# Kernel optimization log

Hardware: AMD Instinct MI355X
Metric: run time of the kernel (lower is better)

## Reference

```python
import jax, jax.numpy as jnp
import numpy as np

B, T, N, D, H, MH = 4, 16, 128, 16, 64, 128  # batch, timesteps, nodes, n_in_node, n_hid, msg_hid


def setup_inputs() -> dict:
    key = jax.random.key(0)
    ks = jax.random.split(key, 24)
    s = 0.1
    inp = {
        'A': jax.random.uniform(ks[0], (B, N, N), dtype=jnp.float32),
        'X': jax.random.normal(ks[1], (B, T, N, D), dtype=jnp.float32),
        'W_msg1': s * jax.random.normal(ks[2], (2 * H, MH), dtype=jnp.float32),
        'b_msg1': s * jax.random.normal(ks[3], (MH,), dtype=jnp.float32),
        'W_msg2': s * jax.random.normal(ks[4], (MH, H), dtype=jnp.float32),
        'b_msg2': s * jax.random.normal(ks[5], (H,), dtype=jnp.float32),
        'W_ir': s * jax.random.normal(ks[6], (D, H), dtype=jnp.float32),
        'b_ir': s * jax.random.normal(ks[7], (H,), dtype=jnp.float32),
        'W_ii': s * jax.random.normal(ks[8], (D, H), dtype=jnp.float32),
        'b_ii': s * jax.random.normal(ks[9], (H,), dtype=jnp.float32),
        'W_in': s * jax.random.normal(ks[10], (D, H), dtype=jnp.float32),
        'b_in': s * jax.random.normal(ks[11], (H,), dtype=jnp.float32),
        'W_hr': s * jax.random.normal(ks[12], (H, H), dtype=jnp.float32),
        'W_hi': s * jax.random.normal(ks[13], (H, H), dtype=jnp.float32),
        'W_hh': s * jax.random.normal(ks[14], (H, H), dtype=jnp.float32),
        'W_o1': s * jax.random.normal(ks[15], (H, H), dtype=jnp.float32),
        'b_o1': s * jax.random.normal(ks[16], (H,), dtype=jnp.float32),
        'W_o2': s * jax.random.normal(ks[17], (H, H), dtype=jnp.float32),
        'b_o2': s * jax.random.normal(ks[18], (H,), dtype=jnp.float32),
        'W_o3': s * jax.random.normal(ks[19], (H, D), dtype=jnp.float32),
        'b_o3': s * jax.random.normal(ks[20], (D,), dtype=jnp.float32),
        'log_sigma': jnp.log(jnp.float32(0.1)),
    }
    return inp


def reference(A, X, W_msg1, b_msg1, W_msg2, b_msg2, W_ir, b_ir, W_ii, b_ii,
              W_in, b_in, W_hr, W_hi, W_hh, W_o1, b_o1, W_o2, b_o2, W_o3,
              b_o3, log_sigma):
    Bv, Tv, Nv, Dv = X.shape
    Hv = W_hr.shape[0]
    # project_adjacency: symmetrize, zero diag, clamp to [0,1]
    A = (A + jnp.swapaxes(A, -1, -2)) * 0.5
    A = A * (1.0 - jnp.eye(Nv, dtype=A.dtype))
    A = jnp.clip(A, 0.0, 1.0)
    # split msg_fc1 into sender / receiver halves (cat([senders, receivers]) @ W)
    W1s, W1r = W_msg1[:Hv], W_msg1[Hv:]

    def step(carry, xs):
        hidden, total = carry
        x_t, x_next = xs  # [B,N,D]
        # message passing on hidden state: msg1[b,i,j] = tanh(h_i@W1s + h_j@W1r + b)
        hs = hidden @ W1s                      # [B,N,MH] sender part
        hr = hidden @ W1r + b_msg1             # [B,N,MH] receiver part
        m1 = jnp.tanh(hs[:, :, None, :] + hr[:, None, :, :])  # [B,N,N,MH]
        msg = jnp.tanh(m1 @ W_msg2 + b_msg2)   # [B,N,N,H]
        # weight by soft adjacency, sum over senders i -> agg at receiver j
        agg = jnp.einsum('bij,bijh->bjh', A, msg)  # [B,N,H]
        # GRU-style gating
        r = jax.nn.sigmoid(x_t @ W_ir + b_ir + agg @ W_hr)
        i = jax.nn.sigmoid(x_t @ W_ii + b_ii + agg @ W_hi)
        n = jnp.tanh(x_t @ W_in + b_in + r * (agg @ W_hh))
        hidden_new = (1.0 - i) * n + i * hidden
        # output MLP with residual
        p1 = jax.nn.relu(hidden_new @ W_o1 + b_o1)
        p2 = jax.nn.relu(p1 @ W_o2 + b_o2)
        pred = x_t + (p2 @ W_o3 + b_o3)
        # gaussian log-likelihood
        sigma = jnp.exp(log_sigma)
        mse = jnp.sum((x_next - pred) ** 2)
        const = Nv * Dv * Bv * jnp.log(sigma * jnp.sqrt(2.0 * jnp.pi))
        total = total - (mse / (2.0 * sigma ** 2) + const)
        return (hidden_new, total), pred

    hidden0 = jnp.zeros((Bv, Nv, Hv), dtype=X.dtype)
    xs = (jnp.swapaxes(X[:, :-1], 0, 1), jnp.swapaxes(X[:, 1:], 0, 1))  # time-major
    (_, loglik), preds = jax.lax.scan(step, (hidden0, jnp.float32(0.0)), xs)
    X_pred = jnp.swapaxes(preds, 0, 1)  # [B, T-1, N, D]
    return X_pred, loglik
```

## Files before the change

### kernel.cpp

```cpp
#include <hip/hip_runtime.h>

#define NBLK 512
#define CSCALE 2.8853900817779268f

#define OFF_HS   0
#define OFF_PART 65536
#define OFF_SYNC 66048
#define OFF_BF   66560

#define BW2F  0
#define BWIR  8192
#define BWII  9216
#define BWIN  10240
#define BWHR  11264
#define BWHI  15360
#define BWHH  19456
#define BWO1  23552
#define BWO2  27648
#define BWO3  31744
#define BW1S  32768
#define BW1RT 49152

#define INIT_TOTAL (32768 + 512 + 49152 + 8192)

typedef __attribute__((ext_vector_type(8))) __bf16 bf16x8;
typedef __attribute__((ext_vector_type(4))) float f32x4;
union frag_u { bf16x8 v; unsigned short s[8]; int4 q; };
union ldu { int4 q; unsigned short s[8]; unsigned u[4]; };

__device__ __forceinline__ unsigned short f2b(float x) {
  unsigned int u = __float_as_uint(x);
  u += 0x7fffu + ((u >> 16) & 1u);
  return (unsigned short)(u >> 16);
}
__device__ __forceinline__ float b2f(unsigned short u) {
  return __uint_as_float(((unsigned int)u) << 16);
}
__device__ __forceinline__ float fast_tanh(float x) {
  float e = __builtin_amdgcn_exp2f(x * CSCALE);
  return 1.0f - 2.0f * __builtin_amdgcn_rcpf(e + 1.0f);
}
__device__ __forceinline__ float tanh_pre(float x) {
  float e = __builtin_amdgcn_exp2f(x);
  return 1.0f - 2.0f * __builtin_amdgcn_rcpf(e + 1.0f);
}
__device__ __forceinline__ float fast_sigmoid(float x) {
  float e = __builtin_amdgcn_exp2f(x * -1.4426950408889634f);
  return __builtin_amdgcn_rcpf(1.0f + e);
}
__device__ __forceinline__ unsigned pack_bf2(float lo, float hi) {
  unsigned a = __float_as_uint(lo) + 0x8000u;
  unsigned b = __float_as_uint(hi) + 0x8000u;
  return __builtin_amdgcn_perm(b, a, 0x07060302u);
}
__device__ __forceinline__ void st_coh_u32(unsigned* p, unsigned v) {
  __hip_atomic_store(p, v, __ATOMIC_RELAXED, __HIP_MEMORY_SCOPE_AGENT);
}
__device__ __forceinline__ void st_coh_i32(int* p, int v) {
  __hip_atomic_store(p, v, __ATOMIC_RELAXED, __HIP_MEMORY_SCOPE_AGENT);
}

__global__ void init_kernel(const float* __restrict__ W_msg2,
                            const float* __restrict__ W_ir, const float* __restrict__ W_ii,
                            const float* __restrict__ W_in,
                            const float* __restrict__ W_hr, const float* __restrict__ W_hi,
                            const float* __restrict__ W_hh,
                            const float* __restrict__ W_o1, const float* __restrict__ W_o2,
                            const float* __restrict__ W_o3,
                            const float* __restrict__ W_msg1, float* __restrict__ ws) {
  int idx = blockIdx.x * 256 + threadIdx.x;
  unsigned short* bw = (unsigned short*)(ws + OFF_BF);
  if (idx < 32768) { ws[OFF_HS + idx] = 0.0f; return; }
  idx -= 32768;
  if (idx < 512) { ((int*)(ws + OFF_SYNC))[idx] = 0; return; }
  idx -= 512;
  if (idx < 8192) {
    int f = idx >> 9, l = (idx >> 3) & 63, jj = idx & 7;
    int kc = f >> 2, nt = f & 3;
    int k = kc * 32 + ((l >> 4) << 3) + jj;
    int n = (nt << 4) + (l & 15);
    bw[BW2F + idx] = f2b(W_msg2[k * 64 + n] * CSCALE);
    return;
  }
  idx -= 8192;
  if (idx < 1024) { bw[BWIR + idx] = f2b(W_ir[idx]); return; }
  idx -= 1024;
  if (idx < 1024) { bw[BWII + idx] = f2b(W_ii[idx]); return; }
  idx -= 1024;
  if (idx < 1024) { bw[BWIN + idx] = f2b(W_in[idx]); return; }
  idx -= 1024;
  if (idx < 4096) { bw[BWHR + idx] = f2b(W_hr[idx]); return; }
  idx -= 4096;
  if (idx < 4096) { bw[BWHI + idx] = f2b(W_hi[idx]); return; }
  idx -= 4096;
  if (idx < 4096) { bw[BWHH + idx] = f2b(W_hh[idx]); return; }
  idx -= 4096;
  if (idx < 4096) { bw[BWO1 + idx] = f2b(W_o1[idx]); return; }
  idx -= 4096;
  if (idx < 4096) { bw[BWO2 + idx] = f2b(W_o2[idx]); return; }
  idx -= 4096;
  if (idx < 1024) { bw[BWO3 + idx] = f2b(W_o3[idx]); return; }
  idx -= 1024;
  if (idx < 16384) { bw[BW1S + idx] = f2b(W_msg1[idx]); return; }
  idx -= 16384;
  if (idx < 8192) {
    int m = idx >> 6, h = idx & 63;
    bw[BW1RT + idx] = f2b(W_msg1[(64 + h) * 128 + m]);
    return;
  }
}

__launch_bounds__(256, 2)
__global__ void step_all_kernel(const float* __restrict__ A, const float* __restrict__ X,
                                const float* __restrict__ b_msg1, const float* __restrict__ b_msg2,
                                const float* __restrict__ b_ir, const float* __restrict__ b_ii,
                                const float* __restrict__ b_in,
                                const float* __restrict__ b_o1, const float* __restrict__ b_o2,
                                const float* __restrict__ b_o3,
                                float* __restrict__ ws, float* __restrict__ out) {
  const int tid = threadIdx.x;
  const int bj = blockIdx.x;
  const int b = bj >> 7, j = bj & 127;
  const int wave = tid >> 6, lane = tid & 63;
  const unsigned short* bw = (const unsigned short*)(ws + OFF_BF);
  unsigned short* hs16 = (unsigned short*)(ws + OFF_HS);
  int* flags = (int*)(ws + OFF_SYNC);

  __shared__ __align__(16) unsigned short lds_gate_t[12288];
  __shared__ __align__(16) unsigned short lds_w1t[8192];
  __shared__ __align__(16) unsigned short lds_outt[9216];
  __shared__ __align__(16) float sh_hr[128];
  __shared__ __align__(16) float sh_Ar[128];
  __shared__ __align__(16) float sh_aggw[4][64];
  __shared__ __align__(16) float sh_agg[64];
  __shared__ __align__(16) float sh_xall[256];
  __shared__ __align__(16) float sh_hid[64];
  __shared__ __align__(16) float sh_hist[960];
  __shared__ __align__(16) float sh_pre[4][64];
  __shared__ int sh_w01;

  for (int i = tid; i < 12288; i += 256) {
    int g = i >> 12, r = i & 4095, c = r >> 8, rem = r & 255, h = rem >> 2, s = rem & 3;
    lds_gate_t[i] = bw[BWHR + (g << 12) + (((c << 2) + s) << 6) + h];
  }
  for (int i = tid; i < 8192; i += 256) {
    int c = i >> 9, rem = i & 511, m = rem >> 2, s = rem & 3;
    lds_w1t[i] = bw[BW1S + (((c << 2) + s) << 7) + m];
  }
  for (int i = tid; i < 8192; i += 256) {
    int o = i >> 12, r = i & 4095, c = r >> 8, rem = r & 255, h = rem >> 2, s = rem & 3;
    lds_outt[i] = bw[BWO1 + (o << 12) + (((c << 2) + s) << 6) + h];
  }
  for (int i = tid; i < 1024; i += 256) {
    int c = i >> 6, rem = i & 63, d = rem >> 2, s = rem & 3;
    lds_outt[8192 + i] = bw[BWO3 + (((c << 2) + s) << 4) + d];
  }
  {
    int t0 = tid >> 4, d = tid & 15;
    sh_xall[tid] = X[(((b << 4) + t0) << 11) + (j << 4) + d];
  }
  if (tid < 128) {
    float a1 = A[(b << 14) + (j << 7) + tid];
    float a2 = A[(b << 14) + (tid << 7) + j];
    float v = 0.5f * (a1 + a2);
    v = (tid == j) ? 0.0f : v;
    sh_Ar[tid] = fminf(fmaxf(v, 0.0f), 1.0f);
    sh_hr[tid] = b_msg1[tid] * CSCALE;
  } else if (tid < 192) {
    sh_hid[tid - 128] = 0.0f;
  }
  if (tid == 0) sh_w01 = 0;

  frag_u Bf[16];
  const int4* bw2 = (const int4*)bw;
#pragma unroll
  for (int f = 0; f < 16; ++f) Bf[f].q = bw2[f * 64 + lane];
  float b2v[4];
#pragma unroll
  for (int nt = 0; nt < 4; ++nt) b2v[nt] = b_msg2[nt * 16 + (lane & 15)] * CSCALE;
  float my_bias = 0.0f;
  float wx[16];
  if (wave != 2) {
    my_bias = (wave == 0) ? b_ir[lane] : (wave == 1) ? b_ii[lane] : b_in[lane];
    const int xo = (wave == 0) ? BWIR : (wave == 1) ? BWII : BWIN;
#pragma unroll
    for (int d = 0; d < 16; ++d) wx[d] = b2f(bw[xo + d * 64 + lane]);
  }
  const float bm1a = b_msg1[lane], bm1b = b_msg1[lane + 64];
  const float bo1 = b_o1[lane], bo2 = b_o2[lane];
  const float bo3 = (lane < 16) ? b_o3[lane] : 0.0f;
  float macc = 0.0f;

  const int lane15 = lane & 15;
  const int k0 = (lane >> 4) << 3;
  __syncthreads();

  for (int t = 0; t < 15; ++t) {
    const int par = t & 1;
    const unsigned short* hs_cur = hs16 + par * 65536;
    unsigned short* hs_nxt = hs16 + (par ^ 1) * 65536;

    ldu va[8];
    {
      const unsigned short* p0 = hs_cur + (((b << 7) + (wave << 5) + lane15) << 7) + k0;
      const unsigned short* p1 = p0 + 2048;
      asm volatile(
          "global_load_dwordx4 %0, %8, off sc0 sc1\n\t"
          "global_load_dwordx4 %1, %8, off offset:64 sc0 sc1\n\t"
          "global_load_dwordx4 %2, %8, off offset:128 sc0 sc1\n\t"
          "global_load_dwordx4 %3, %8, off offset:192 sc0 sc1\n\t"
          "global_load_dwordx4 %4, %9, off sc0 sc1\n\t"
          "global_load_dwordx4 %5, %9, off offset:64 sc0 sc1\n\t"
          "global_load_dwordx4 %6, %9, off offset:128 sc0 sc1\n\t"
          "global_load_dwordx4 %7, %9, off offset:192 sc0 sc1\n\t"
          "s_waitcnt vmcnt(0)"
          : "=&v"(va[0].q), "=&v"(va[1].q), "=&v"(va[2].q), "=&v"(va[3].q),
            "=&v"(va[4].q), "=&v"(va[5].q), "=&v"(va[6].q), "=&v"(va[7].q)
          : "v"(p0), "v"(p1)
          : "memory");
    }

    float part[4] = {0.f, 0.f, 0.f, 0.f};
#pragma unroll
    for (int c = 0; c < 2; ++c) {
      f32x4 acc[4];
#pragma unroll
      for (int nt = 0; nt < 4; ++nt) acc[nt] = (f32x4){0.f, 0.f, 0.f, 0.f};
#pragma unroll
      for (int kc = 0; kc < 4; ++kc) {
        const ldu& u = va[c * 4 + kc];
        const float* hp = sh_hr + kc * 32 + k0;
        frag_u Af;
        int* ap = (int*)&Af.q;
#pragma unroll
        for (int p = 0; p < 4; ++p) {
          unsigned w = u.u[p];
          float x0 = __uint_as_float(w << 16) + hp[2 * p];
          float x1 = __uint_as_float(w & 0xffff0000u) + hp[2 * p + 1];
          ap[p] = (int)pack_bf2(tanh_pre(x0), tanh_pre(x1));
        }
#pragma unroll
        for (int nt = 0; nt < 4; ++nt)
          acc[nt] = __builtin_amdgcn_mfma_f32_16x16x32_bf16(Af.v, Bf[kc * 4 + nt].v, acc[nt], 0, 0, 0);
      }
      const int ibase = ((wave << 1) + c) << 4;
      float4 aw = *(const float4*)(sh_Ar + ibase + ((lane >> 4) << 2));
#pragma unroll
      for (int r = 0; r < 4; ++r) {
        float wv = (r == 0) ? aw.x : (r == 1) ? aw.y : (r == 2) ? aw.z : aw.w;
#pragma unroll
        for (int nt = 0; nt < 4; ++nt)
          part[nt] += wv * tanh_pre(acc[nt][r] + b2v[nt]);
      }
    }
#pragma unroll
    for (int nt = 0; nt < 4; ++nt) {
      part[nt] += __shfl_xor(part[nt], 16);
      part[nt] += __shfl_xor(part[nt], 32);
    }
    if (lane < 16) {
#pragma unroll
      for (int nt = 0; nt < 4; ++nt) sh_aggw[wave][nt * 16 + lane] = part[nt];
    }
    __syncthreads();
    if (tid < 64)
      sh_agg[tid] = sh_aggw[0][tid] + sh_aggw[1][tid] + sh_aggw[2][tid] + sh_aggw[3][tid];
    __syncthreads();

    {
      float s = 0.0f;
      if (wave != 2) {
        s = my_bias;
        const float4* xr = (const float4*)(sh_xall + (t << 4));
#pragma unroll
        for (int c = 0; c < 4; ++c) {
          float4 xv = xr[c];
          s += xv.x * wx[4 * c] + xv.y * wx[4 * c + 1] + xv.z * wx[4 * c + 2] + xv.w * wx[4 * c + 3];
        }
      }
      if (wave != 3) {
        const ushort4* gp = ((const ushort4*)lds_gate_t) + (wave << 10) + lane;
        const float4* ag = (const float4*)sh_agg;
        float a0 = s, a1 = 0.f, a2 = 0.f, a3 = 0.f;
#pragma unroll
        for (int c = 0; c < 16; ++c) {
          ushort4 wv = gp[c << 6];
          float4 av = ag[c];
          a0 += av.x * b2f(wv.x); a1 += av.y * b2f(wv.y);
          a2 += av.z * b2f(wv.z); a3 += av.w * b2f(wv.w);
        }
        s = (a0 + a1) + (a2 + a3);
      }
      sh_pre[wave][lane] = s;
    }
    __syncthreads();
    if (tid < 64) {
      float r  = fast_sigmoid(sh_pre[0][tid]);
      float ig = fast_sigmoid(sh_pre[1][tid]);
      float n  = fast_tanh(sh_pre[3][tid] + r * sh_pre[2][tid]);
      float hnew = (1.0f - ig) * n + ig * sh_hid[tid];
      sh_hid[tid] = hnew;
      sh_hist[t * 64 + tid] = hnew;
    }
    __syncthreads();

    if (t < 14) {
      if (wave <= 1) {
        const int m = tid;
        const ushort4* wp = ((const ushort4*)lds_w1t) + m;
        const float4* h4 = (const float4*)sh_hid;
        float a0 = 0.f, a1 = 0.f, a2 = 0.f, a3 = 0.f;
#pragma unroll
        for (int c = 0; c < 16; ++c) {
          ushort4 wv = wp[c << 7];
          float4 hv = h4[c];
          a0 += hv.x * b2f(wv.x); a1 += hv.y * b2f(wv.y);
          a2 += hv.z * b2f(wv.z); a3 += hv.w * b2f(wv.w);
        }
        float s = ((a0 + a1) + (a2 + a3)) * CSCALE;
        float hi = __shfl_down(s, 1);
        if (!(lane & 1))
          st_coh_u32((unsigned*)hs_nxt + (bj << 6) + (m >> 1), pack_bf2(s, hi));
        asm volatile("s_waitcnt vmcnt(0)" ::: "memory");
        if (lane == 0) atomicAdd(&sh_w01, 1);
        if (wave == 0) {
          const int tgt = t + 1;
          if (lane == 0) {
            while (__hip_atomic_load(&sh_w01, __ATOMIC_RELAXED, __HIP_MEMORY_SCOPE_WORKGROUP) < 2 * tgt) {}
            st_coh_i32(flags + (b << 7) + j, tgt);
          }
          const int* fp = flags + (b << 7) + (lane << 1);
          int2 fv;
          for (;;) {
            asm volatile("global_load_dwordx2 %0, %1, off sc0 sc1\n\ts_waitcnt vmcnt(0)"
                         : "=v"(fv) : "v"(fp) : "memory");
            if (!__any(fv.x < tgt || fv.y < tgt)) break;
            __builtin_amdgcn_s_sleep(1);
          }
        }
      } else if (wave == 2) {
        const int4* wp1 = (const int4*)(bw + BW1RT + (lane << 6));
        const int4* wp2 = (const int4*)(bw + BW1RT + ((lane + 64) << 6));
        const float4* h4 = (const float4*)sh_hid;
        float s1a = bm1a, s1b = 0.f, s2a = bm1b, s2b = 0.f;
#pragma unroll
        for (int c = 0; c < 8; ++c) {
          ldu u1, u2; u1.q = wp1[c]; u2.q = wp2[c];
          float4 h0 = h4[2 * c], h1 = h4[2 * c + 1];
          s1a += h0.x * b2f(u1.s[0]); s1b += h0.y * b2f(u1.s[1]);
          s1a += h0.z * b2f(u1.s[2]); s1b += h0.w * b2f(u1.s[3]);
          s1a += h1.x * b2f(u1.s[4]); s1b += h1.y * b2f(u1.s[5]);
          s1a += h1.z * b2f(u1.s[6]); s1b += h1.w * b2f(u1.s[7]);
          s2a += h0.x * b2f(u2.s[0]); s2b += h0.y * b2f(u2.s[1]);
          s2a += h0.z * b2f(u2.s[2]); s2b += h0.w * b2f(u2.s[3]);
          s2a += h1.x * b2f(u2.s[4]); s2b += h1.y * b2f(u2.s[5]);
          s2a += h1.z * b2f(u2.s[6]); s2b += h1.w * b2f(u2.s[7]);
        }
        sh_hr[lane] = (s1a + s1b) * CSCALE;
        sh_hr[lane + 64] = (s2a + s2b) * CSCALE;
      }
    }
    __syncthreads();
  }

#pragma unroll
  for (int it = 0; it < 4; ++it) {
    const int tt = wave + it * 4;
    if (tt >= 15) continue;
    const float4* h4 = (const float4*)(sh_hist + tt * 64);
    {
      const ushort4* r1 = ((const ushort4*)lds_outt) + lane;
      float a0 = bo1, a1 = 0.f, a2 = 0.f, a3 = 0.f;
#pragma unroll
      for (int c = 0; c < 16; ++c) {
        ushort4 wv = r1[c << 6]; float4 hv = h4[c];
        a0 += hv.x * b2f(wv.x); a1 += hv.y * b2f(wv.y);
        a2 += hv.z * b2f(wv.z); a3 += hv.w * b2f(wv.w);
      }
      sh_pre[wave][lane] = fmaxf((a0 + a1) + (a2 + a3), 0.0f);
    }
    {
      const ushort4* r2 = ((const ushort4*)lds_outt) + 1024 + lane;
      const float4* p4 = (const float4*)sh_pre[wave];
      float a0 = bo2, a1 = 0.f, a2 = 0.f, a3 = 0.f;
#pragma unroll
      for (int c = 0; c < 16; ++c) {
        ushort4 wv = r2[c << 6]; float4 pv = p4[c];
        a0 += pv.x * b2f(wv.x); a1 += pv.y * b2f(wv.y);
        a2 += pv.z * b2f(wv.z); a3 += pv.w * b2f(wv.w);
      }
      sh_aggw[wave][lane] = fmaxf((a0 + a1) + (a2 + a3), 0.0f);
    }
    if (lane < 16) {
      const ushort4* r3 = ((const ushort4*)lds_outt) + 2048 + lane;
      const float4* q4 = (const float4*)sh_aggw[wave];
      float a0 = bo3, a1 = 0.f, a2 = 0.f, a3 = 0.f;
#pragma unroll
      for (int c = 0; c < 16; ++c) {
        ushort4 wv = r3[c << 4]; float4 qv = q4[c];
        a0 += qv.x * b2f(wv.x); a1 += qv.y * b2f(wv.y);
        a2 += qv.z * b2f(wv.z); a3 += qv.w * b2f(wv.w);
      }
      float pred = sh_xall[(tt << 4) + lane] + (a0 + a1) + (a2 + a3);
      out[((b * 15 + tt) * 128 + j) * 16 + lane] = pred;
      float d = sh_xall[((tt + 1) << 4) + lane] - pred;
      macc += d * d;
    }
  }
  macc += __shfl_xor(macc, 1);
  macc += __shfl_xor(macc, 2);
  macc += __shfl_xor(macc, 4);
  macc += __shfl_xor(macc, 8);
  __syncthreads();
  if (lane == 0) sh_agg[wave] = macc;
  __syncthreads();
  if (tid == 0) ws[OFF_PART + bj] = sh_agg[0] + sh_agg[1] + sh_agg[2] + sh_agg[3];
}

__global__ void final_kernel(const float* __restrict__ log_sigma, const float* __restrict__ ws,
                             float* __restrict__ out) {
  __shared__ float red[256];
  const int tid = threadIdx.x;
  red[tid] = ws[OFF_PART + tid] + ws[OFF_PART + 256 + tid];
  __syncthreads();
  if (tid == 0) {
    float mse = 0.0f;
    for (int i = 0; i < 256; ++i) mse += red[i];
    float sigma = expf(log_sigma[0]);
    float cst = 8192.0f * logf(sigma * sqrtf(6.2831853071795864f));
    out[122880] = -(mse / (2.0f * sigma * sigma) + 15.0f * cst);
  }
}

extern "C" void kernel_launch(void* const* d_in, const int* in_sizes, int n_in,
                              void* d_out, int out_size, void* d_ws, size_t ws_size,
                              hipStream_t stream) {
  (void)in_sizes; (void)n_in; (void)out_size; (void)ws_size;
  const float* A      = (const float*)d_in[0];
  const float* X      = (const float*)d_in[1];
  const float* W_msg1 = (const float*)d_in[2];
  const float* b_msg1 = (const float*)d_in[3];
  const float* W_msg2 = (const float*)d_in[4];
  const float* b_msg2 = (const float*)d_in[5];
  const float* W_ir   = (const float*)d_in[6];
  const float* b_ir   = (const float*)d_in[7];
  const float* W_ii   = (const float*)d_in[8];
  const float* b_ii   = (const float*)d_in[9];
  const float* W_in   = (const float*)d_in[10];
  const float* b_in   = (const float*)d_in[11];
  const float* W_hr   = (const float*)d_in[12];
  const float* W_hi   = (const float*)d_in[13];
  const float* W_hh   = (const float*)d_in[14];
  const float* W_o1   = (const float*)d_in[15];
  const float* b_o1   = (const float*)d_in[16];
  const float* W_o2   = (const float*)d_in[17];
  const float* b_o2   = (const float*)d_in[18];
  const float* W_o3   = (const float*)d_in[19];
  const float* b_o3   = (const float*)d_in[20];
  const float* log_sigma = (const float*)d_in[21];
  float* ws  = (float*)d_ws;
  float* out = (float*)d_out;

  init_kernel<<<(INIT_TOTAL + 255) / 256, 256, 0, stream>>>(
      W_msg2, W_ir, W_ii, W_in, W_hr, W_hi, W_hh, W_o1, W_o2, W_o3, W_msg1, ws);
  step_all_kernel<<<NBLK, 256, 0, stream>>>(A, X, b_msg1, b_msg2, b_ir, b_ii, b_in,
                                            b_o1, b_o2, b_o3, ws, out);
  final_kernel<<<1, 256, 0, stream>>>(log_sigma, ws, out);
}
```

Baseline: 273.7 us.

## Replace per-block flag polling with hierarchical atomic-counter barrier and remap block indices

The per-batch inter-block barrier used to have every block publish a flag and then poll all 128 peer flags with wide coherent loads. It is replaced by a two-level counter tree: 8 padded leaf counters of 16 blocks each, a root counter, and a single release flag per batch and timestep, so each block polls only one word. The block-to-(batch, node) mapping is also permuted so that batches interleave across block IDs in groups of 64. The intent is to cut polling traffic and barrier latency, at the cost of a serial chain of atomics and a larger zero-initialised sync region.

```diff
diff --git a/kernel.cpp b/kernel.cpp
--- a/kernel.cpp
+++ b/kernel.cpp
@@ -6,7 +6,10 @@
 #define OFF_HS   0
 #define OFF_PART 65536
 #define OFF_SYNC 66048
-#define OFF_BF   66560
+#define OFF_BF   85248
+
+#define SYNC_ROOT 15360
+#define SYNC_FLAG 17280
 
 #define BW2F  0
 #define BWIR  8192
@@ -21,7 +24,7 @@
 #define BW1S  32768
 #define BW1RT 49152
 
-#define INIT_TOTAL (32768 + 512 + 49152 + 8192)
+#define INIT_TOTAL (32768 + 19200 + 49152 + 8192)
 
 typedef __attribute__((ext_vector_type(8))) __bf16 bf16x8;
 typedef __attribute__((ext_vector_type(4))) float f32x4;
@@ -72,8 +75,8 @@
   unsigned short* bw = (unsigned short*)(ws + OFF_BF);
   if (idx < 32768) { ws[OFF_HS + idx] = 0.0f; return; }
   idx -= 32768;
-  if (idx < 512) { ((int*)(ws + OFF_SYNC))[idx] = 0; return; }
-  idx -= 512;
+  if (idx < 19200) { ((int*)(ws + OFF_SYNC))[idx] = 0; return; }
+  idx -= 19200;
   if (idx < 8192) {
     int f = idx >> 9, l = (idx >> 3) & 63, jj = idx & 7;
     int kc = f >> 2, nt = f & 3;
@@ -120,11 +123,13 @@
                                 float* __restrict__ ws, float* __restrict__ out) {
   const int tid = threadIdx.x;
   const int bj = blockIdx.x;
-  const int b = bj >> 7, j = bj & 127;
+  const int b = (bj >> 6) & 3;
+  const int j = (bj & 63) | ((bj >> 8) << 6);
+  const int row = (b << 7) + j;
   const int wave = tid >> 6, lane = tid & 63;
   const unsigned short* bw = (const unsigned short*)(ws + OFF_BF);
   unsigned short* hs16 = (unsigned short*)(ws + OFF_HS);
-  int* flags = (int*)(ws + OFF_SYNC);
+  int* sync = (int*)(ws + OFF_SYNC);
 
   __shared__ __align__(16) unsigned short lds_gate_t[12288];
   __shared__ __align__(16) unsigned short lds_w1t[8192];
@@ -320,23 +325,24 @@
         float s = ((a0 + a1) + (a2 + a3)) * CSCALE;
         float hi = __shfl_down(s, 1);
         if (!(lane & 1))
-          st_coh_u32((unsigned*)hs_nxt + (bj << 6) + (m >> 1), pack_bf2(s, hi));
+          st_coh_u32((unsigned*)hs_nxt + (row << 6) + (m >> 1), pack_bf2(s, hi));
         asm volatile("s_waitcnt vmcnt(0)" ::: "memory");
         if (lane == 0) atomicAdd(&sh_w01, 1);
-        if (wave == 0) {
+        if (wave == 0 && lane == 0) {
           const int tgt = t + 1;
-          if (lane == 0) {
-            while (__hip_atomic_load(&sh_w01, __ATOMIC_RELAXED, __HIP_MEMORY_SCOPE_WORKGROUP) < 2 * tgt) {}
-            st_coh_i32(flags + (b << 7) + j, tgt);
+          while (__hip_atomic_load(&sh_w01, __ATOMIC_RELAXED, __HIP_MEMORY_SCOPE_WORKGROUP) < 2 * tgt) {}
+          const int bt = b * 15 + t;
+          int* leaf = sync + ((bt << 3) + (j & 7)) * 32;
+          int* root = sync + SYNC_ROOT + bt * 32;
+          int* flag = sync + SYNC_FLAG + bt * 32;
+          int r = __hip_atomic_fetch_add(leaf, 1, __ATOMIC_RELAXED, __HIP_MEMORY_SCOPE_AGENT);
+          if (r == 15) {
+            int r2 = __hip_atomic_fetch_add(root, 1, __ATOMIC_RELAXED, __HIP_MEMORY_SCOPE_AGENT);
+            if (r2 == 7)
+              __hip_atomic_store(flag, 1, __ATOMIC_RELAXED, __HIP_MEMORY_SCOPE_AGENT);
           }
-          const int* fp = flags + (b << 7) + (lane << 1);
-          int2 fv;
-          for (;;) {
-            asm volatile("global_load_dwordx2 %0, %1, off sc0 sc1\n\ts_waitcnt vmcnt(0)"
-                         : "=v"(fv) : "v"(fp) : "memory");
-            if (!__any(fv.x < tgt || fv.y < tgt)) break;
+          while (__hip_atomic_load(flag, __ATOMIC_RELAXED, __HIP_MEMORY_SCOPE_AGENT) == 0)
             __builtin_amdgcn_s_sleep(1);
-          }
         }
       } else if (wave == 2) {
         const int4* wp1 = (const int4*)(bw + BW1RT + (lane << 6));
```

After: 246.9 us. -9.8%, faster.
